# Optimization experiments

Measured on AMD Instinct MI355X. Metric: run time of the kernel, lower is better.

## Reference

```python
import jax, jax.numpy as jnp
import numpy as np

N = 100000   # nodes
E = 2000000  # edges per etype
D = 256      # in_dim
C = 16       # num_classes (per-etype Linear out dim)
R = 4        # number of canonical etypes


def setup_inputs() -> dict:
    key = jax.random.key(0)
    k0, k1, k2, k3, k4, k5 = jax.random.split(key, 6)
    feat = jax.random.normal(k0, (N, D), dtype=jnp.float32)
    src_idx = jax.random.randint(k1, (R, E), 0, N, dtype=jnp.int32)
    dst_idx = jax.random.randint(k2, (R, E), 0, N, dtype=jnp.int32)
    eweight = jax.random.uniform(k3, (R, E, 1), dtype=jnp.float32)
    W = jax.random.normal(k4, (R, D, C), dtype=jnp.float32) / np.sqrt(D).astype(np.float32)
    b = jax.random.normal(k5, (R, C), dtype=jnp.float32) * 0.01
    return {"feat": feat, "src_idx": src_idx, "dst_idx": dst_idx,
            "eweight": eweight, "W": W, "b": b}


def reference(feat, src_idx, dst_idx, eweight, W, b):
    """Hetero GNN layer: per-etype Linear -> u_mul_e message -> mean reduce per
    dst node -> sum across etypes (DGL multi_update_all(..., 'sum'))."""
    n = feat.shape[0]

    def per_etype(Wr, br, src, dst, ew):
        wh = feat @ Wr + br                      # [N, C] per-etype linear
        m = jnp.take(wh, src, axis=0) * ew       # [E, C] u_mul_e message
        s = jax.ops.segment_sum(m, dst, num_segments=n)            # [N, C]
        cnt = jax.ops.segment_sum(jnp.ones((src.shape[0],), feat.dtype),
                                  dst, num_segments=n)             # [N]
        # DGL mean: nodes with no incoming messages contribute 0
        cnt = cnt[:, None]
        return jnp.where(cnt > 0, s / jnp.maximum(cnt, 1.0), jnp.zeros_like(s))

    h = jax.vmap(per_etype)(W, b, src_idx, dst_idx, eweight)  # [R, N, C]
    return h.sum(axis=0)                                       # cross-etype sum
```

## Files before the change

kernel.cpp:

```cpp
#include <hip/hip_runtime.h>

constexpr int N = 100000;
constexpr int E = 2000000;
constexpr int D = 256;
constexpr int C = 16;
constexpr int R = 4;
constexpr int NCOL = R * C;
constexpr int TOT = R * E;

constexpr int BKN = 256;
constexpr int NBUK = (N + BKN - 1) / BKN;
constexpr int EPB = 16384;
constexpr int NBLK = (E + EPB - 1) / EPB;
constexpr int NROWS = R * NBUK;
constexpr int HLEN = NROWS * NBLK;
constexpr int SCAN_ELEMS = 2048;
constexpr int SCAN_NBLK = (HLEN + SCAN_ELEMS - 1) / SCAN_ELEMS;
constexpr int CAP = 3328;
constexpr int CHK = 4096;
constexpr int AGRID = ((NBUK + 1) / 2) * 8;
constexpr int SGRID = ((NBLK + 1) / 2) * 8;

typedef __attribute__((ext_vector_type(8))) short short8;
typedef __attribute__((ext_vector_type(8))) unsigned short u16x8;
typedef __attribute__((ext_vector_type(4))) float f32x4;
typedef __attribute__((ext_vector_type(4))) int i32x4;

__device__ __forceinline__ float bf2f(unsigned short h) {
    return __uint_as_float(((unsigned int)h) << 16);
}
__device__ __forceinline__ unsigned short f2bf(float f) {
    unsigned int x = __float_as_uint(f);
    x += 0x7FFFu + ((x >> 16) & 1u);
    return (unsigned short)(x >> 16);
}

__global__ void wt_kernel(const float* __restrict__ W, short8* __restrict__ wtb) {
    const int idx = blockIdx.x * blockDim.x + threadIdx.x;
    if (idx >= 8 * 4 * 64) return;
    const int lane = idx & 63;
    const int ct   = (idx >> 6) & 3;
    const int ks   = idx >> 8;
    const int r = ct, c = lane & 15;
    const int kbase = ks * 32 + (lane >> 4) * 8;
    short8 v;
#pragma unroll
    for (int j = 0; j < 8; ++j)
        v[j] = (short)f2bf(W[(size_t)r * D * C + (size_t)(kbase + j) * C + c]);
    wtb[idx] = v;
}

__global__ __launch_bounds__(256) void gemm_kernel(
    const f32x4* __restrict__ feat4, const short8* __restrict__ wtb,
    const float* __restrict__ b, unsigned short* __restrict__ whb) {
    __shared__ unsigned short alds[64 * 272];
    const int t   = threadIdx.x;
    const int n0  = blockIdx.x * 64;

#pragma unroll
    for (int j = 0; j < 16; ++j) {
        const int idx = t + j * 256;
        const int row = idx >> 6, k4 = idx & 63;
        const int grow = n0 + row;
        const int lrow = (grow < N) ? grow : (N - 1);
        const f32x4 v = __builtin_nontemporal_load(&feat4[(size_t)lrow * 64 + k4]);
        ushort4 u;
        u.x = f2bf(v.x); u.y = f2bf(v.y); u.z = f2bf(v.z); u.w = f2bf(v.w);
        *(ushort4*)&alds[row * 272 + k4 * 4] = u;
    }
    __syncthreads();

    const int lane = t & 63;
    const int wv   = t >> 6;
    const int wrow = wv * 16 + (lane & 15);
    const int kblk = lane >> 4;

    f32x4 acc0 = {0.f, 0.f, 0.f, 0.f};
    f32x4 acc1 = acc0, acc2 = acc0, acc3 = acc0;

#pragma unroll
    for (int ks = 0; ks < 8; ++ks) {
        const short8 af = *(const short8*)&alds[wrow * 272 + ks * 32 + kblk * 8];
        const short8 b0 = wtb[(ks * 4 + 0) * 64 + lane];
        const short8 b1 = wtb[(ks * 4 + 1) * 64 + lane];
        const short8 b2 = wtb[(ks * 4 + 2) * 64 + lane];
        const short8 b3 = wtb[(ks * 4 + 3) * 64 + lane];
        acc0 = __builtin_amdgcn_mfma_f32_16x16x32_bf16(af, b0, acc0, 0, 0, 0);
        acc1 = __builtin_amdgcn_mfma_f32_16x16x32_bf16(af, b1, acc1, 0, 0, 0);
        acc2 = __builtin_amdgcn_mfma_f32_16x16x32_bf16(af, b2, acc2, 0, 0, 0);
        acc3 = __builtin_amdgcn_mfma_f32_16x16x32_bf16(af, b3, acc3, 0, 0, 0);
    }

    const int c    = lane & 15;
    const int rowb = n0 + wv * 16 + (lane >> 4) * 4;
    const float bias0 = b[ 0 + c];
    const float bias1 = b[16 + c];
    const float bias2 = b[32 + c];
    const float bias3 = b[48 + c];
#pragma unroll
    for (int reg = 0; reg < 4; ++reg) {
        const int gr = rowb + reg;
        if (gr < N) {
            whb[((size_t)0 * N + gr) * 16 + c] = f2bf(acc0[reg] + bias0);
            whb[((size_t)1 * N + gr) * 16 + c] = f2bf(acc1[reg] + bias1);
            whb[((size_t)2 * N + gr) * 16 + c] = f2bf(acc2[reg] + bias2);
            whb[((size_t)3 * N + gr) * 16 + c] = f2bf(acc3[reg] + bias3);
        }
    }
}

__global__ __launch_bounds__(256) void hist_kernel(const int* __restrict__ dst,
                                                   int* __restrict__ hist) {
    __shared__ int hcnt[NBUK];
    const int t = threadIdx.x;
    const int r = blockIdx.y;
    for (int i = t; i < NBUK; i += 256) hcnt[i] = 0;
    __syncthreads();
    const int e0 = blockIdx.x * EPB;
    if (E - e0 >= EPB) {
        const i32x4* d4 = (const i32x4*)(dst + (size_t)r * E + e0);
#pragma unroll
        for (int j = 0; j < EPB / 1024; ++j) {
            const i32x4 d = __builtin_nontemporal_load(&d4[t + j * 256]);
            atomicAdd(&hcnt[d.x >> 8], 1);
            atomicAdd(&hcnt[d.y >> 8], 1);
            atomicAdd(&hcnt[d.z >> 8], 1);
            atomicAdd(&hcnt[d.w >> 8], 1);
        }
    } else {
        const int* d = dst + (size_t)r * E;
        for (int e = e0 + t; e < E; e += 256)
            atomicAdd(&hcnt[d[e] >> 8], 1);
    }
    __syncthreads();
    for (int i = t; i < NBUK; i += 256)
        hist[(size_t)(r * NBUK + i) * NBLK + blockIdx.x] = hcnt[i];
}

__global__ __launch_bounds__(256) void scan1_kernel(int* __restrict__ data,
                                                    int* __restrict__ partials) {
    __shared__ int sh[256];
    const int t = threadIdx.x;
    const int idx = blockIdx.x * SCAN_ELEMS + t * 8;
    int v[8];
#pragma unroll
    for (int j = 0; j < 8; ++j)
        v[j] = (idx + j < HLEN) ? data[idx + j] : 0;
    int s = 0;
#pragma unroll
    for (int j = 0; j < 8; ++j) s += v[j];
    sh[t] = s;
    __syncthreads();
    for (int off = 1; off < 256; off <<= 1) {
        int x = (t >= off) ? sh[t - off] : 0;
        __syncthreads();
        sh[t] += x;
        __syncthreads();
    }
    int run = sh[t] - s;
    if (t == 255) partials[blockIdx.x] = sh[255];
#pragma unroll
    for (int j = 0; j < 8; ++j) {
        if (idx + j < HLEN) data[idx + j] = run;
        run += v[j];
    }
}

__global__ __launch_bounds__(1024) void scan2_kernel(int* __restrict__ partials, int n) {
    __shared__ int sh[1024];
    const int t = threadIdx.x;
    int a = (2 * t     < n) ? partials[2 * t]     : 0;
    int b = (2 * t + 1 < n) ? partials[2 * t + 1] : 0;
    const int s = a + b;
    sh[t] = s;
    __syncthreads();
    for (int off = 1; off < 1024; off <<= 1) {
        int x = (t >= off) ? sh[t - off] : 0;
        __syncthreads();
        sh[t] += x;
        __syncthreads();
    }
    const int excl = sh[t] - s;
    if (2 * t     < n) partials[2 * t]     = excl;
    if (2 * t + 1 < n) partials[2 * t + 1] = excl + a;
}

__global__ void scan3_kernel(int* __restrict__ data, const int* __restrict__ partials) {
    const int i = blockIdx.x * blockDim.x + threadIdx.x;
    if (i < HLEN) data[i] += partials[i / SCAN_ELEMS];
}

__global__ __launch_bounds__(512) void scatter_kernel(const int* __restrict__ src,
                                                      const int* __restrict__ dst,
                                                      const float* __restrict__ ew,
                                                      const int* __restrict__ hist,
                                                      int2* __restrict__ sorted) {
    __shared__ int2 lrec[CHK];
    __shared__ int  lidx[CHK];
    __shared__ short lbkt[CHK];
    __shared__ int gcur[NBUK];
    __shared__ int loff[NBUK + 1];
    __shared__ int lcnt[NBUK];
    const int t = threadIdx.x;
    const int s = blockIdx.x & 7;
    const int r = s >> 1;
    const int cb0 = (blockIdx.x >> 3) * 2 + (s & 1);
    if (cb0 >= NBLK) return;

    for (int i = t; i < NBUK; i += 512)
        gcur[i] = hist[(size_t)(r * NBUK + i) * NBLK + cb0];

    const int e0 = cb0 * EPB;
    const int e1 = min(e0 + EPB, E);
    const int* sp = src + (size_t)r * E;
    const int* dp = dst + (size_t)r * E;
    const float* wp = ew + (size_t)r * E;

    for (int cb = e0; cb < e1; cb += CHK) {
        const int L = min(CHK, e1 - cb);
        for (int i = t; i < NBUK; i += 512) lcnt[i] = 0;
        __syncthreads();

        if (L == CHK) {
            const i32x4* s4 = (const i32x4*)(sp + cb);
            const i32x4* d4 = (const i32x4*)(dp + cb);
            const f32x4* w4 = (const f32x4*)(wp + cb);
#pragma unroll
            for (int j = 0; j < CHK / 2048; ++j) {
                const int v = t + j * 512;
                const i32x4 d = __builtin_nontemporal_load(&d4[v]);
                const i32x4 s2 = __builtin_nontemporal_load(&s4[v]);
                const f32x4 w = __builtin_nontemporal_load(&w4[v]);
#pragma unroll
                for (int q = 0; q < 4; ++q) {
                    const int dd = (q == 0) ? d.x : (q == 1) ? d.y : (q == 2) ? d.z : d.w;
                    const int ss = (q == 0) ? s2.x : (q == 1) ? s2.y : (q == 2) ? s2.z : s2.w;
                    const float ww = (q == 0) ? w.x : (q == 1) ? w.y : (q == 2) ? w.z : w.w;
                    const int b = dd >> 8;
                    int2 p;
                    p.x = ss | ((dd & 255) << 20);
                    p.y = __float_as_int(ww);
                    lrec[v * 4 + q] = p;
                    lbkt[v * 4 + q] = (short)b;
                    atomicAdd(&lcnt[b], 1);
                }
            }
        } else {
            for (int i = t; i < L; i += 512) {
                const int dd = dp[cb + i];
                const int ss = sp[cb + i];
                const float ww = wp[cb + i];
                const int b = dd >> 8;
                int2 p;
                p.x = ss | ((dd & 255) << 20);
                p.y = __float_as_int(ww);
                lrec[i] = p;
                lbkt[i] = (short)b;
                atomicAdd(&lcnt[b], 1);
            }
        }
        __syncthreads();

        for (int off = 1; off < NBUK; off <<= 1) {
            int x = 0;
            if (t < NBUK && t >= off) x = lcnt[t - off];
            __syncthreads();
            if (t < NBUK) lcnt[t] += x;
            __syncthreads();
        }
        if (t < NBUK) loff[t + 1] = lcnt[t];
        if (t == 0) loff[0] = 0;
        __syncthreads();
        if (t < NBUK) lcnt[t] = loff[t];
        __syncthreads();

        for (int i = t; i < L; i += 512) {
            const int b = lbkt[i];
            const int pos = atomicAdd(&lcnt[b], 1);
            lidx[pos] = i | (b << 16);
        }
        __syncthreads();

        for (int p = t; p < L; p += 512) {
            const int v = lidx[p];
            const int i = v & 0xFFFF;
            const int b = v >> 16;
            sorted[gcur[b] + (p - loff[b])] = lrec[i];
        }
        __syncthreads();

        for (int b = t; b < NBUK; b += 512)
            gcur[b] += loff[b + 1] - loff[b];
        __syncthreads();
    }
}

__global__ __launch_bounds__(512) void accum_kernel(const int2* __restrict__ sorted,
                                                    const u16x8* __restrict__ whb8,
                                                    const int* __restrict__ hist,
                                                    float* __restrict__ part) {
    __shared__ int2 lrec[CAP];
    __shared__ unsigned short lidx[CAP];
    __shared__ float tile[BKN * 16];
    __shared__ int degs[BKN];
    __shared__ int loff[BKN + 1];
    __shared__ int lcur[BKN];
    __shared__ int nextg;
    const int t = threadIdx.x;
    const int s  = blockIdx.x & 7;
    const int r  = s >> 1;
    const int ck = (blockIdx.x >> 3) * 2 + (s & 1);
    if (ck >= NBUK) return;
    const int lane = t & 63;
    const int h = t & 1;

    const int row = r * NBUK + ck;
    const int start = hist[(size_t)row * NBLK];
    const int end   = (row + 1 < NROWS) ? hist[(size_t)(row + 1) * NBLK] : TOT;
    const int L = end - start;
    int L0 = (L + 1) >> 1; if (L0 > CAP) L0 = CAP;
    int L1 = L - L0;       if (L1 > CAP) L1 = CAP;

    const int wbase = r * N;

    for (int i = t; i < BKN * 16; i += 512) tile[i] = 0.f;
    if (t < BKN) degs[t] = 0;

    int pbase = start;
    int plen  = L0;
#pragma unroll
    for (int pass = 0; pass < 2; ++pass) {
        if (t < BKN) lcur[t] = 0;
        if (t == 0) nextg = 0;
        __syncthreads();

        for (int i = t; i < plen; i += 512) {
            long long raw = __builtin_nontemporal_load((const long long*)&sorted[pbase + i]);
            int2 p = *(int2*)&raw;
            lrec[i] = p;
            atomicAdd(&lcur[(p.x >> 20) & 255], 1);
        }
        __syncthreads();

        if (t < 64) {
            const int b0 = lcur[4 * t], b1 = lcur[4 * t + 1];
            const int b2 = lcur[4 * t + 2], b3 = lcur[4 * t + 3];
            const int ssum = b0 + b1 + b2 + b3;
            int incl = ssum;
#pragma unroll
            for (int off = 1; off < 64; off <<= 1) {
                const int x = __shfl_up(incl, off, 64);
                if (t >= off) incl += x;
            }
            const int excl = incl - ssum;
            loff[4 * t]     = excl;                lcur[4 * t]     = excl;
            loff[4 * t + 1] = excl + b0;           lcur[4 * t + 1] = excl + b0;
            loff[4 * t + 2] = excl + b0 + b1;      lcur[4 * t + 2] = excl + b0 + b1;
            loff[4 * t + 3] = excl + b0 + b1 + b2; lcur[4 * t + 3] = excl + b0 + b1 + b2;
            if (t == 63) loff[BKN] = incl;
        }
        __syncthreads();

        for (int i = t; i < plen; i += 512) {
            const int dl = (lrec[i].x >> 20) & 255;
            const int pos = atomicAdd(&lcur[dl], 1);
            lidx[pos] = (unsigned short)i;
        }
        __syncthreads();

        const int evenlane = lane & ~1;
        while (true) {
            int n = 0;
            if (h == 0) n = atomicAdd(&nextg, 1);
            n = __shfl(n, evenlane, 64);
            const bool active = (n < BKN);
            if (__all(!active)) break;
            if (active) {
                const int s0 = loff[n], e0 = loff[n + 1];

                float a0 = 0.f, a1 = 0.f, a2 = 0.f, a3 = 0.f;
                float a4 = 0.f, a5 = 0.f, a6 = 0.f, a7 = 0.f;
                int j = s0;
                for (; j + 4 <= e0; j += 4) {
                    const int i0 = lidx[j], i1 = lidx[j + 1];
                    const int i2 = lidx[j + 2], i3 = lidx[j + 3];
                    const int2 r0 = lrec[i0], r1 = lrec[i1], r2 = lrec[i2], r3 = lrec[i3];
                    const u16x8 u0 = whb8[(size_t)(wbase + (r0.x & 0xFFFFF)) * 2 + h];
                    const u16x8 u1 = whb8[(size_t)(wbase + (r1.x & 0xFFFFF)) * 2 + h];
                    const u16x8 u2 = whb8[(size_t)(wbase + (r2.x & 0xFFFFF)) * 2 + h];
                    const u16x8 u3 = whb8[(size_t)(wbase + (r3.x & 0xFFFFF)) * 2 + h];
                    const float w0 = __int_as_float(r0.y), w1 = __int_as_float(r1.y);
                    const float w2 = __int_as_float(r2.y), w3 = __int_as_float(r3.y);
                    a0 += bf2f(u0[0]) * w0 + bf2f(u1[0]) * w1 + bf2f(u2[0]) * w2 + bf2f(u3[0]) * w3;
                    a1 += bf2f(u0[1]) * w0 + bf2f(u1[1]) * w1 + bf2f(u2[1]) * w2 + bf2f(u3[1]) * w3;
                    a2 += bf2f(u0[2]) * w0 + bf2f(u1[2]) * w1 + bf2f(u2[2]) * w2 + bf2f(u3[2]) * w3;
                    a3 += bf2f(u0[3]) * w0 + bf2f(u1[3]) * w1 + bf2f(u2[3]) * w2 + bf2f(u3[3]) * w3;
                    a4 += bf2f(u0[4]) * w0 + bf2f(u1[4]) * w1 + bf2f(u2[4]) * w2 + bf2f(u3[4]) * w3;
                    a5 += bf2f(u0[5]) * w0 + bf2f(u1[5]) * w1 + bf2f(u2[5]) * w2 + bf2f(u3[5]) * w3;
                    a6 += bf2f(u0[6]) * w0 + bf2f(u1[6]) * w1 + bf2f(u2[6]) * w2 + bf2f(u3[6]) * w3;
                    a7 += bf2f(u0[7]) * w0 + bf2f(u1[7]) * w1 + bf2f(u2[7]) * w2 + bf2f(u3[7]) * w3;
                }
                for (; j < e0; ++j) {
                    const int2 r0 = lrec[lidx[j]];
                    const u16x8 u0 = whb8[(size_t)(wbase + (r0.x & 0xFFFFF)) * 2 + h];
                    const float w0 = __int_as_float(r0.y);
                    a0 += bf2f(u0[0]) * w0; a1 += bf2f(u0[1]) * w0;
                    a2 += bf2f(u0[2]) * w0; a3 += bf2f(u0[3]) * w0;
                    a4 += bf2f(u0[4]) * w0; a5 += bf2f(u0[5]) * w0;
                    a6 += bf2f(u0[6]) * w0; a7 += bf2f(u0[7]) * w0;
                }

                float* tp = &tile[n * 16 + h * 8];
                float4 v0 = *(float4*)tp;
                float4 v1 = *(float4*)(tp + 4);
                v0.x += a0; v0.y += a1; v0.z += a2; v0.w += a3;
                v1.x += a4; v1.y += a5; v1.z += a6; v1.w += a7;
                *(float4*)tp = v0;
                *(float4*)(tp + 4) = v1;
                if (h == 0) degs[n] += e0 - s0;
            }
        }
        __syncthreads();

        pbase += plen;
        plen = L1;
    }

    const int g2 = t >> 1;
    const int node = ck * BKN + g2;
    if (node < N) {
        const int deg = degs[g2];
        const float inv = (deg > 0) ? 1.f / (float)deg : 0.f;
        const float* tp = &tile[g2 * 16 + h * 8];
        float4 v0, v1;
        v0.x = tp[0] * inv; v0.y = tp[1] * inv; v0.z = tp[2] * inv; v0.w = tp[3] * inv;
        v1.x = tp[4] * inv; v1.y = tp[5] * inv; v1.z = tp[6] * inv; v1.w = tp[7] * inv;
        float* op = &part[(size_t)(wbase + node) * 16 + h * 8];
        *(float4*)op = v0;
        *(float4*)(op + 4) = v1;
    }
}

__global__ void finalize_kernel(const float4* __restrict__ part4,
                                float4* __restrict__ out4) {
    const int i = blockIdx.x * blockDim.x + threadIdx.x;
    if (i >= N * 4) return;
    float4 a = part4[i];
    const float4 b = part4[(size_t)N * 4 + i];
    const float4 c = part4[(size_t)2 * N * 4 + i];
    const float4 d = part4[(size_t)3 * N * 4 + i];
    a.x += b.x + c.x + d.x;
    a.y += b.y + c.y + d.y;
    a.z += b.z + c.z + d.z;
    a.w += b.w + c.w + d.w;
    out4[i] = a;
}

extern "C" void kernel_launch(void* const* d_in, const int* in_sizes, int n_in,
                              void* d_out, int out_size, void* d_ws, size_t ws_size,
                              hipStream_t stream) {
    const float* feat = (const float*)d_in[0];
    const int*   src  = (const int*)d_in[1];
    const int*   dst  = (const int*)d_in[2];
    const float* ew   = (const float*)d_in[3];
    const float* W    = (const float*)d_in[4];
    const float* b    = (const float*)d_in[5];
    float* out = (float*)d_out;

    char* base = (char*)d_ws;
    int2*           sorted   = (int2*)base;           base += (size_t)TOT * 8;
    short8*         wtb      = (short8*)base;         base += (size_t)64 * NCOL * 16;
    unsigned short* whb      = (unsigned short*)base; base += (size_t)R * N * C * 2;
    int*            hist     = (int*)base;            base += (size_t)HLEN * 4;
    int*            partials = (int*)base;            base += (size_t)4096;
    float*          part     = (float*)base;

    wt_kernel<<<8, 256, 0, stream>>>(W, wtb);
    gemm_kernel<<<(N + 63) / 64, 256, 0, stream>>>((const f32x4*)feat, wtb, b, whb);

    hist_kernel<<<dim3(NBLK, R), 256, 0, stream>>>(dst, hist);
    scan1_kernel<<<SCAN_NBLK, 256, 0, stream>>>(hist, partials);
    scan2_kernel<<<1, 1024, 0, stream>>>(partials, SCAN_NBLK);
    scan3_kernel<<<(HLEN + 255) / 256, 256, 0, stream>>>(hist, partials);

    scatter_kernel<<<SGRID, 512, 0, stream>>>(src, dst, ew, hist, sorted);
    accum_kernel<<<AGRID, 512, 0, stream>>>(sorted, (const u16x8*)whb, hist, part);
    finalize_kernel<<<(N * 4 + 255) / 256, 256, 0, stream>>>((const float4*)part, (float4*)out);
}
```

Before: 176.4 us.

## Merge GEMM and histogram launches; use wave-shuffle scan for local bucket offsets

The GEMM and destination-histogram kernels become one launch in which the block index selects the role, so the two independent stages can run concurrently and one launch is removed. The histogram reuses the GEMM's shared-memory buffer. Separately, the scatter kernel's per-block bucket prefix sum changes from a barrier-heavy Hillis-Steele loop to a single-wavefront scan: each lane sums 7 bins and the lanes combine with shuffles. The shared-memory footprint of histogram blocks rises to the GEMM's, which may reduce occupancy for those blocks.

```diff
diff --git a/kernel.cpp b/kernel.cpp
--- a/kernel.cpp
+++ b/kernel.cpp
@@ -20,6 +20,7 @@
 constexpr int CHK = 4096;
 constexpr int AGRID = ((NBUK + 1) / 2) * 8;
 constexpr int SGRID = ((NBLK + 1) / 2) * 8;
+constexpr int GEMMB = (N + 63) / 64;
 
 typedef __attribute__((ext_vector_type(8))) short short8;
 typedef __attribute__((ext_vector_type(8))) unsigned short u16x8;
@@ -50,91 +51,92 @@
     wtb[idx] = v;
 }
 
-__global__ __launch_bounds__(256) void gemm_kernel(
+__global__ __launch_bounds__(256) void gemmhist_kernel(
     const f32x4* __restrict__ feat4, const short8* __restrict__ wtb,
-    const float* __restrict__ b, unsigned short* __restrict__ whb) {
+    const float* __restrict__ b, unsigned short* __restrict__ whb,
+    const int* __restrict__ dst, int* __restrict__ hist) {
     __shared__ unsigned short alds[64 * 272];
-    const int t   = threadIdx.x;
-    const int n0  = blockIdx.x * 64;
-
-#pragma unroll
-    for (int j = 0; j < 16; ++j) {
-        const int idx = t + j * 256;
-        const int row = idx >> 6, k4 = idx & 63;
-        const int grow = n0 + row;
-        const int lrow = (grow < N) ? grow : (N - 1);
-        const f32x4 v = __builtin_nontemporal_load(&feat4[(size_t)lrow * 64 + k4]);
-        ushort4 u;
-        u.x = f2bf(v.x); u.y = f2bf(v.y); u.z = f2bf(v.z); u.w = f2bf(v.w);
-        *(ushort4*)&alds[row * 272 + k4 * 4] = u;
-    }
-    __syncthreads();
-
-    const int lane = t & 63;
-    const int wv   = t >> 6;
-    const int wrow = wv * 16 + (lane & 15);
-    const int kblk = lane >> 4;
-
-    f32x4 acc0 = {0.f, 0.f, 0.f, 0.f};
-    f32x4 acc1 = acc0, acc2 = acc0, acc3 = acc0;
-
-#pragma unroll
-    for (int ks = 0; ks < 8; ++ks) {
-        const short8 af = *(const short8*)&alds[wrow * 272 + ks * 32 + kblk * 8];
-        const short8 b0 = wtb[(ks * 4 + 0) * 64 + lane];
-        const short8 b1 = wtb[(ks * 4 + 1) * 64 + lane];
-        const short8 b2 = wtb[(ks * 4 + 2) * 64 + lane];
-        const short8 b3 = wtb[(ks * 4 + 3) * 64 + lane];
-        acc0 = __builtin_amdgcn_mfma_f32_16x16x32_bf16(af, b0, acc0, 0, 0, 0);
-        acc1 = __builtin_amdgcn_mfma_f32_16x16x32_bf16(af, b1, acc1, 0, 0, 0);
-        acc2 = __builtin_amdgcn_mfma_f32_16x16x32_bf16(af, b2, acc2, 0, 0, 0);
-        acc3 = __builtin_amdgcn_mfma_f32_16x16x32_bf16(af, b3, acc3, 0, 0, 0);
-    }
-
-    const int c    = lane & 15;
-    const int rowb = n0 + wv * 16 + (lane >> 4) * 4;
-    const float bias0 = b[ 0 + c];
-    const float bias1 = b[16 + c];
-    const float bias2 = b[32 + c];
-    const float bias3 = b[48 + c];
-#pragma unroll
-    for (int reg = 0; reg < 4; ++reg) {
-        const int gr = rowb + reg;
-        if (gr < N) {
-            whb[((size_t)0 * N + gr) * 16 + c] = f2bf(acc0[reg] + bias0);
-            whb[((size_t)1 * N + gr) * 16 + c] = f2bf(acc1[reg] + bias1);
-            whb[((size_t)2 * N + gr) * 16 + c] = f2bf(acc2[reg] + bias2);
-            whb[((size_t)3 * N + gr) * 16 + c] = f2bf(acc3[reg] + bias3);
-        }
-    }
-}
-
-__global__ __launch_bounds__(256) void hist_kernel(const int* __restrict__ dst,
-                                                   int* __restrict__ hist) {
-    __shared__ int hcnt[NBUK];
     const int t = threadIdx.x;
-    const int r = blockIdx.y;
-    for (int i = t; i < NBUK; i += 256) hcnt[i] = 0;
-    __syncthreads();
-    const int e0 = blockIdx.x * EPB;
-    if (E - e0 >= EPB) {
-        const i32x4* d4 = (const i32x4*)(dst + (size_t)r * E + e0);
-#pragma unroll
-        for (int j = 0; j < EPB / 1024; ++j) {
-            const i32x4 d = __builtin_nontemporal_load(&d4[t + j * 256]);
-            atomicAdd(&hcnt[d.x >> 8], 1);
-            atomicAdd(&hcnt[d.y >> 8], 1);
-            atomicAdd(&hcnt[d.z >> 8], 1);
-            atomicAdd(&hcnt[d.w >> 8], 1);
+
+    if (blockIdx.x < GEMMB) {
+        const int n0 = blockIdx.x * 64;
+#pragma unroll
+        for (int j = 0; j < 16; ++j) {
+            const int idx = t + j * 256;
+            const int row = idx >> 6, k4 = idx & 63;
+            const int grow = n0 + row;
+            const int lrow = (grow < N) ? grow : (N - 1);
+            const f32x4 v = __builtin_nontemporal_load(&feat4[(size_t)lrow * 64 + k4]);
+            ushort4 u;
+            u.x = f2bf(v.x); u.y = f2bf(v.y); u.z = f2bf(v.z); u.w = f2bf(v.w);
+            *(ushort4*)&alds[row * 272 + k4 * 4] = u;
+        }
+        __syncthreads();
+
+        const int lane = t & 63;
+        const int wv   = t >> 6;
+        const int wrow = wv * 16 + (lane & 15);
+        const int kblk = lane >> 4;
+
+        f32x4 acc0 = {0.f, 0.f, 0.f, 0.f};
+        f32x4 acc1 = acc0, acc2 = acc0, acc3 = acc0;
+
+#pragma unroll
+        for (int ks = 0; ks < 8; ++ks) {
+            const short8 af = *(const short8*)&alds[wrow * 272 + ks * 32 + kblk * 8];
+            const short8 b0 = wtb[(ks * 4 + 0) * 64 + lane];
+            const short8 b1 = wtb[(ks * 4 + 1) * 64 + lane];
+            const short8 b2 = wtb[(ks * 4 + 2) * 64 + lane];
+            const short8 b3 = wtb[(ks * 4 + 3) * 64 + lane];
+            acc0 = __builtin_amdgcn_mfma_f32_16x16x32_bf16(af, b0, acc0, 0, 0, 0);
+            acc1 = __builtin_amdgcn_mfma_f32_16x16x32_bf16(af, b1, acc1, 0, 0, 0);
+            acc2 = __builtin_amdgcn_mfma_f32_16x16x32_bf16(af, b2, acc2, 0, 0, 0);
+            acc3 = __builtin_amdgcn_mfma_f32_16x16x32_bf16(af, b3, acc3, 0, 0, 0);
+        }
+
+        const int c    = lane & 15;
+        const int rowb = n0 + wv * 16 + (lane >> 4) * 4;
+        const float bias0 = b[ 0 + c];
+        const float bias1 = b[16 + c];
+        const float bias2 = b[32 + c];
+        const float bias3 = b[48 + c];
+#pragma unroll
+        for (int reg = 0; reg < 4; ++reg) {
+            const int gr = rowb + reg;
+            if (gr < N) {
+                whb[((size_t)0 * N + gr) * 16 + c] = f2bf(acc0[reg] + bias0);
+                whb[((size_t)1 * N + gr) * 16 + c] = f2bf(acc1[reg] + bias1);
+                whb[((size_t)2 * N + gr) * 16 + c] = f2bf(acc2[reg] + bias2);
+                whb[((size_t)3 * N + gr) * 16 + c] = f2bf(acc3[reg] + bias3);
+            }
         }
     } else {
-        const int* d = dst + (size_t)r * E;
-        for (int e = e0 + t; e < E; e += 256)
-            atomicAdd(&hcnt[d[e] >> 8], 1);
-    }
-    __syncthreads();
-    for (int i = t; i < NBUK; i += 256)
-        hist[(size_t)(r * NBUK + i) * NBLK + blockIdx.x] = hcnt[i];
+        int* hcnt = (int*)alds;
+        const int q  = blockIdx.x - GEMMB;
+        const int r  = q / NBLK;
+        const int cb = q - r * NBLK;
+        for (int i = t; i < NBUK; i += 256) hcnt[i] = 0;
+        __syncthreads();
+        const int e0 = cb * EPB;
+        if (E - e0 >= EPB) {
+            const i32x4* d4 = (const i32x4*)(dst + (size_t)r * E + e0);
+#pragma unroll
+            for (int j = 0; j < EPB / 1024; ++j) {
+                const i32x4 d = __builtin_nontemporal_load(&d4[t + j * 256]);
+                atomicAdd(&hcnt[d.x >> 8], 1);
+                atomicAdd(&hcnt[d.y >> 8], 1);
+                atomicAdd(&hcnt[d.z >> 8], 1);
+                atomicAdd(&hcnt[d.w >> 8], 1);
+            }
+        } else {
+            const int* d = dst + (size_t)r * E;
+            for (int e = e0 + t; e < E; e += 256)
+                atomicAdd(&hcnt[d[e] >> 8], 1);
+        }
+        __syncthreads();
+        for (int i = t; i < NBUK; i += 256)
+            hist[(size_t)(r * NBUK + i) * NBLK + cb] = hcnt[i];
+    }
 }
 
 __global__ __launch_bounds__(256) void scan1_kernel(int* __restrict__ data,
@@ -261,17 +263,30 @@
         }
         __syncthreads();
 
-        for (int off = 1; off < NBUK; off <<= 1) {
-            int x = 0;
-            if (t < NBUK && t >= off) x = lcnt[t - off];
-            __syncthreads();
-            if (t < NBUK) lcnt[t] += x;
-            __syncthreads();
-        }
-        if (t < NBUK) loff[t + 1] = lcnt[t];
-        if (t == 0) loff[0] = 0;
-        __syncthreads();
-        if (t < NBUK) lcnt[t] = loff[t];
+        if (t < 64) {
+            int bv[7];
+            int ssum = 0;
+#pragma unroll
+            for (int j = 0; j < 7; ++j) {
+                const int bin = 7 * t + j;
+                bv[j] = (bin < NBUK) ? lcnt[bin] : 0;
+                ssum += bv[j];
+            }
+            int incl = ssum;
+#pragma unroll
+            for (int off = 1; off < 64; off <<= 1) {
+                const int x = __shfl_up(incl, off, 64);
+                if (t >= off) incl += x;
+            }
+            int run = incl - ssum;
+#pragma unroll
+            for (int j = 0; j < 7; ++j) {
+                const int bin = 7 * t + j;
+                if (bin < NBUK) { loff[bin] = run; lcnt[bin] = run; }
+                run += bv[j];
+            }
+            if (t == 63) loff[NBUK] = incl;
+        }
         __syncthreads();
 
         for (int i = t; i < L; i += 512) {
@@ -476,9 +491,9 @@
     float*          part     = (float*)base;
 
     wt_kernel<<<8, 256, 0, stream>>>(W, wtb);
-    gemm_kernel<<<(N + 63) / 64, 256, 0, stream>>>((const f32x4*)feat, wtb, b, whb);
-
-    hist_kernel<<<dim3(NBLK, R), 256, 0, stream>>>(dst, hist);
+    gemmhist_kernel<<<GEMMB + R * NBLK, 256, 0, stream>>>(
+        (const f32x4*)feat, wtb, b, whb, dst, hist);
+
     scan1_kernel<<<SCAN_NBLK, 256, 0, stream>>>(hist, partials);
     scan2_kernel<<<1, 1024, 0, stream>>>(partials, SCAN_NBLK);
     scan3_kernel<<<(HLEN + 255) / 256, 256, 0, stream>>>(hist, partials);
```

After: 178.0 us. Within noise of the previous version (+0.9%).
